# Performance work log

Hardware: AMD Instinct MI355X
Metric: run time of the kernel (lower is better)

## Reference

```python
import jax, jax.numpy as jnp
import numpy as np

DIM = 1024
NUM_HEADS = 16
HEAD_DIM = DIM // NUM_HEADS
EPS = 1e-5


def setup_inputs() -> dict:
    key = jax.random.key(0)
    ks = jax.random.split(key, 8)
    B, N = 4, 2048
    s = 0.02
    return {
        "x1": jax.random.normal(ks[0], (B, N, DIM), jnp.float32),
        "x2": jax.random.normal(ks[1], (B, N, DIM), jnp.float32),
        "wq": jax.random.normal(ks[2], (DIM, DIM), jnp.float32) * s,
        "bq": jnp.zeros((DIM,), jnp.float32),
        "wkv": jax.random.normal(ks[3], (DIM, 2 * DIM), jnp.float32) * s,
        "bkv": jnp.zeros((2 * DIM,), jnp.float32),
        "gamma_q": jnp.ones((HEAD_DIM,), jnp.float32),
        "beta_q": jnp.zeros((HEAD_DIM,), jnp.float32),
        "gamma_k": jnp.ones((HEAD_DIM,), jnp.float32),
        "beta_k": jnp.zeros((HEAD_DIM,), jnp.float32),
    }


def _layernorm(x, gamma, beta):
    m = jnp.mean(x, axis=-1, keepdims=True)
    v = jnp.mean(jnp.square(x - m), axis=-1, keepdims=True)
    return (x - m) * jax.lax.rsqrt(v + EPS) * gamma + beta


def reference(x1, x2, wq, bq, wkv, bkv, gamma_q, beta_q, gamma_k, beta_k):
    B, N, C = x1.shape
    H, D = NUM_HEADS, C // NUM_HEADS
    q = x1 @ wq + bq                      # [B,N,C]
    kv = x2 @ wkv + bkv                   # [B,N,2C]
    k, v = kv[..., :C], kv[..., C:]
    # [B,N,C] -> [B,H,N,D]
    q = q.reshape(B, N, H, D).transpose(0, 2, 1, 3)
    k = k.reshape(B, N, H, D).transpose(0, 2, 1, 3)
    v = v.reshape(B, N, H, D).transpose(0, 2, 1, 3)
    q = _layernorm(q, gamma_q, beta_q)
    k = _layernorm(k, gamma_k, beta_k)
    scale = 1.0 / jnp.sqrt(jnp.asarray(D, x1.dtype))
    scores = jnp.einsum("bhnd,bhmd->bhnm", q, k) * scale
    attn = jax.nn.softmax(scores, axis=-1)
    out = jnp.einsum("bhnm,bhmd->bhnd", attn, v)  # [B,H,N,D]
    return out.transpose(0, 2, 1, 3).reshape(B, N, C)
```

## Files before the change

### kernel.cpp

```cpp
#include <hip/hip_runtime.h>
#include <hip/hip_bf16.h>

#define NHEADS 16
#define HDIM 64
#define BATCH 4
#define SEQ 2048
#define CDIM 1024
#define ROWS (BATCH * SEQ)
#define QSCALE (0.125f * 1.44269504088896f)

typedef __attribute__((ext_vector_type(8))) short short8;
typedef __attribute__((ext_vector_type(4))) float f32x4;
typedef __attribute__((ext_vector_type(4))) unsigned int u32x4;
typedef __attribute__((ext_vector_type(2))) unsigned int u32x2;

__device__ inline short f2bf(float f) {
    unsigned int u = __builtin_bit_cast(unsigned int, f);
    unsigned int r = (u + 0x7fffu + ((u >> 16) & 1u)) >> 16;
    return (short)r;
}

__device__ __forceinline__ void gll16(const void* g, void* l) {
    __builtin_amdgcn_global_load_lds(
        (const __attribute__((address_space(1))) unsigned int*)g,
        (__attribute__((address_space(3))) unsigned int*)l, 16, 0, 0);
}

__device__ __forceinline__ unsigned int pack_bf2(float a, float b) {
    return __builtin_amdgcn_perm(__builtin_bit_cast(unsigned int, b),
                                 __builtin_bit_cast(unsigned int, a), 0x07060302u);
}

__global__ __launch_bounds__(256) void cvt_bf16(const float* __restrict__ src,
                                                short* __restrict__ dst, int n8) {
    int i = blockIdx.x * 256 + threadIdx.x;
    if (i < n8) {
        f32x4 a = ((const f32x4*)src)[i * 2];
        f32x4 b = ((const f32x4*)src)[i * 2 + 1];
        short8 o;
        o[0] = f2bf(a[0]); o[1] = f2bf(a[1]); o[2] = f2bf(a[2]); o[3] = f2bf(a[3]);
        o[4] = f2bf(b[0]); o[5] = f2bf(b[1]); o[6] = f2bf(b[2]); o[7] = f2bf(b[3]);
        ((short8*)dst)[i] = o;
    }
}

__global__ __launch_bounds__(256) void wtrans(const float* __restrict__ W,
                                              short* __restrict__ WT, int Nw) {
    __shared__ short T[64][72];
    const int t = threadIdx.x;
    const int n0 = blockIdx.x * 64, k0 = blockIdx.y * 64;
    const int kl = t >> 2, c4 = (t & 3) * 16;
    const float* src = W + (size_t)(k0 + kl) * Nw + n0 + c4;
    short8 s0, s1;
#pragma unroll
    for (int e = 0; e < 2; e++) {
        f32x4 u = *(const f32x4*)(src + e * 4);
        s0[e * 4 + 0] = f2bf(u[0]); s0[e * 4 + 1] = f2bf(u[1]);
        s0[e * 4 + 2] = f2bf(u[2]); s0[e * 4 + 3] = f2bf(u[3]);
        f32x4 v = *(const f32x4*)(src + 8 + e * 4);
        s1[e * 4 + 0] = f2bf(v[0]); s1[e * 4 + 1] = f2bf(v[1]);
        s1[e * 4 + 2] = f2bf(v[2]); s1[e * 4 + 3] = f2bf(v[3]);
    }
    *(short8*)&T[kl][c4] = s0;
    *(short8*)&T[kl][c4 + 8] = s1;
    __syncthreads();
#pragma unroll
    for (int pass = 0; pass < 2; pass++) {
        int n = (t >> 3) + pass * 32;
        short8 o;
#pragma unroll
        for (int e = 0; e < 8; e++) o[e] = T[(t & 7) * 8 + e][n];
        *(short8*)(WT + (size_t)(n0 + n) * 1024 + k0 + (t & 7) * 8) = o;
    }
}

__global__ __launch_bounds__(256) void gemm_fused(
    const short* __restrict__ A1,
    const short* __restrict__ A2,
    const short* __restrict__ WQT,
    const short* __restrict__ WKVT,
    const float* __restrict__ bq,
    const float* __restrict__ bkv,
    const float* __restrict__ gq, const float* __restrict__ btq,
    const float* __restrict__ gk, const float* __restrict__ btk,
    short* __restrict__ QOut,
    short* __restrict__ KOut,
    short* __restrict__ VT)
{
    __shared__ __align__(16) char smem[34816];
    short (*As)[32] = (short (*)[32])smem;
    short (*Bs)[32] = (short (*)[32])(smem + 8192);

    const int tid = threadIdx.x;
    const int wave = tid >> 6, lane = tid & 63;
    const int wr = wave >> 1, wc = wave & 1;
    const int quad = lane >> 4, l15 = lane & 15;

    const int lin = blockIdx.y * 24 + blockIdx.x;
    const int swz = (lin & 7) * 192 + (lin >> 3);
    const int rblk = swz / 24;
    const int cblkg = swz - rblk * 24;

    const bool isQ = cblkg < 8;
    const int cblk = isQ ? cblkg : cblkg - 8;
    const short* Ap = isQ ? A1 : A2;
    const short* BT = isQ ? WQT : WKVT;

    f32x4 acc[4][4];
#pragma unroll
    for (int i = 0; i < 4; i++)
#pragma unroll
        for (int j = 0; j < 4; j++) acc[i][j] = f32x4{0.f, 0.f, 0.f, 0.f};

    const int srow = wave * 32 + (lane >> 2);
    const int scol = (lane & 3) * 8;

    for (int k0 = 0; k0 < CDIM; k0 += 32) {
        __syncthreads();
#pragma unroll
        for (int c = 0; c < 2; c++) {
            gll16(Ap + (size_t)(rblk * 128 + srow + c * 16) * CDIM + k0 + scol,
                  &As[srow + c * 16][scol]);
            gll16(BT + (size_t)(cblk * 128 + srow + c * 16) * CDIM + k0 + scol,
                  &Bs[srow + c * 16][scol]);
        }
        __syncthreads();

        short8 af[4], bfr[4];
#pragma unroll
        for (int i = 0; i < 4; i++)
            af[i] = *(const short8*)&As[wr * 64 + i * 16 + l15][quad * 8];
#pragma unroll
        for (int j = 0; j < 4; j++)
            bfr[j] = *(const short8*)&Bs[wc * 64 + j * 16 + l15][quad * 8];
#pragma unroll
        for (int i = 0; i < 4; i++)
#pragma unroll
            for (int j = 0; j < 4; j++)
                acc[i][j] = __builtin_amdgcn_mfma_f32_16x16x32_bf16(af[i], bfr[j], acc[i][j], 0, 0, 0);
    }

    const int col0 = cblk * 128 + wc * 64;
    const int g = col0 >> 6;

    if (cblkg < 16) {
        const float* bias  = isQ ? bq : bkv;
        const float* gamma = isQ ? gq : gk;
        const float* beta  = isQ ? btq : btk;
        short* Out = isQ ? QOut : KOut;
        const float scale = isQ ? QSCALE : 1.f;
        const int h = g;
        float bv[4], gv[4], btv[4];
#pragma unroll
        for (int j = 0; j < 4; j++) {
            int d = j * 16 + l15;
            bv[j] = bias[col0 + d];
            gv[j] = gamma[d];
            btv[j] = beta[d];
        }
#pragma unroll
        for (int i = 0; i < 4; i++) {
            int rowl = rblk * 128 + wr * 64 + i * 16 + quad * 4;
#pragma unroll
            for (int reg = 0; reg < 4; reg++) {
                float x[4], s = 0.f, s2 = 0.f;
#pragma unroll
                for (int j = 0; j < 4; j++) {
                    x[j] = acc[i][j][reg] + bv[j];
                    s += x[j];
                    s2 += x[j] * x[j];
                }
#pragma unroll
                for (int m = 1; m < 16; m <<= 1) {
                    s += __shfl_xor(s, m);
                    s2 += __shfl_xor(s2, m);
                }
                float mean = s * (1.f / 64.f);
                float var = s2 * (1.f / 64.f) - mean * mean;
                float rstd = rsqrtf(var + 1e-5f);
                int r = rowl + reg;
                int b = r >> 11, n = r & (SEQ - 1);
                size_t base = (((size_t)b * NHEADS + h) * SEQ + n) * 64;
#pragma unroll
                for (int j = 0; j < 4; j++) {
                    float y = ((x[j] - mean) * rstd * gv[j] + btv[j]) * scale;
                    Out[base + j * 16 + l15] = f2bf(y);
                }
            }
        }
    } else {
        const int h = g - NHEADS;
        __syncthreads();
        short (*Ts)[64][68] = (short (*)[64][68])smem;
#pragma unroll
        for (int i = 0; i < 4; i++)
#pragma unroll
            for (int reg = 0; reg < 4; reg++)
#pragma unroll
                for (int j = 0; j < 4; j++)
                    Ts[wave][i * 16 + quad * 4 + reg][j * 16 + l15] =
                        f2bf(acc[i][j][reg] + bkv[col0 + j * 16 + l15]);
        const int r = rblk * 128 + wr * 64 + lane;
        const int b = r >> 11, n = r & (SEQ - 1);
        const size_t vtbase = (((size_t)b * NHEADS + h) * 64) * SEQ;
#pragma unroll
        for (int e8 = 0; e8 < 8; e8++) {
            short8 v = *(const short8*)&Ts[wave][lane][e8 * 8];
#pragma unroll
            for (int e = 0; e < 8; e++)
                VT[vtbase + (size_t)(e8 * 8 + e) * SEQ + n] = v[e];
        }
    }
}

template <int JD, bool FIRST>
__device__ __forceinline__ void band_store(float* __restrict__ Ot,
                                           const f32x4 (&o)[4][4],
                                           int l15, int q) {
#pragma unroll
    for (int qc = 0; qc < 4; qc++)
#pragma unroll
        for (int reg = 0; reg < 4; reg++) {
            float* dst = &Ot[(qc * 16 + l15) * 68 + JD * 16 + q * 4 + reg];
            if (FIRST) *dst = o[JD][qc][reg];
            else       *dst += o[JD][qc][reg];
        }
}

__global__ __launch_bounds__(256, 2) void attn_fa(
    const short* __restrict__ Q,
    const short* __restrict__ Kk,
    const short* __restrict__ VT,
    float* __restrict__ Out)
{
    __shared__ __align__(16) char smem_raw[20480];

    const int tid = threadIdx.x;
    const int w = tid >> 6, lane = tid & 63;
    const int q = lane >> 4, l15 = lane & 15;
    const int bh = blockIdx.x;
    const int b = bh >> 4, h = bh & 15;
    const int qt = blockIdx.y;
    const size_t hb = (size_t)bh * SEQ * 64;
    const size_t vb = (size_t)bh * 64 * SEQ;

    unsigned int* Pd = (unsigned int*)smem_raw + w * 1280;
    float* Ot = (float*)smem_raw;
    float* Lred = (float*)smem_raw + 64 * 68;

    short8 qf[4][2];
#pragma unroll
    for (int qc = 0; qc < 4; qc++)
#pragma unroll
        for (int dh = 0; dh < 2; dh++)
            qf[qc][dh] = *(const short8*)(Q + hb +
                (size_t)(qt * 64 + qc * 16 + l15) * 64 + dh * 32 + q * 8);

    short8 ones;
#pragma unroll
    for (int e = 0; e < 8; e++) ones[e] = (short)0x3F80;

    f32x4 o[4][4];
#pragma unroll
    for (int jd = 0; jd < 4; jd++)
#pragma unroll
        for (int qc = 0; qc < 4; qc++) o[jd][qc] = f32x4{0.f, 0.f, 0.f, 0.f};
    f32x4 osum[4];
#pragma unroll
    for (int qc = 0; qc < 4; qc++) osum[qc] = f32x4{0.f, 0.f, 0.f, 0.f};

    const short* kbase = Kk + hb + (size_t)(w * 32 + l15) * 64 + q * 8;
    const short* vbase = VT + vb + (size_t)l15 * SEQ + w * 32 + q * 8;

    for (int kti = 0; kti < 16; kti++) {
        short8 kf[2][2];
#pragma unroll
        for (int kt = 0; kt < 2; kt++)
#pragma unroll
            for (int dh = 0; dh < 2; dh++)
                kf[kt][dh] = *(const short8*)(kbase +
                    (size_t)(kti * 128 + kt * 16) * 64 + dh * 32);
        short8 vf[4];
#pragma unroll
        for (int jd = 0; jd < 4; jd++)
            vf[jd] = *(const short8*)(vbase + (size_t)(jd * 16) * SEQ + kti * 128);

#pragma unroll
        for (int kt = 0; kt < 2; kt++)
#pragma unroll
            for (int qc = 0; qc < 4; qc++) {
                f32x4 z = f32x4{0.f, 0.f, 0.f, 0.f};
                z = __builtin_amdgcn_mfma_f32_16x16x32_bf16(kf[kt][0], qf[qc][0], z, 0, 0, 0);
                z = __builtin_amdgcn_mfma_f32_16x16x32_bf16(kf[kt][1], qf[qc][1], z, 0, 0, 0);
                u32x2 d2;
                d2[0] = pack_bf2(__builtin_amdgcn_exp2f(z[0]), __builtin_amdgcn_exp2f(z[1]));
                d2[1] = pack_bf2(__builtin_amdgcn_exp2f(z[2]), __builtin_amdgcn_exp2f(z[3]));
                *(u32x2*)&Pd[(qc * 16 + l15) * 20 + kt * 8 + 2 * q] = d2;
            }

        short8 pf[4];
#pragma unroll
        for (int qc = 0; qc < 4; qc++) {
            u32x4 pr = *(const u32x4*)&Pd[(qc * 16 + l15) * 20 + 4 * q];
            pf[qc] = __builtin_bit_cast(short8, pr);
        }

#pragma unroll
        for (int qc = 0; qc < 4; qc++)
            osum[qc] = __builtin_amdgcn_mfma_f32_16x16x32_bf16(ones, pf[qc], osum[qc], 0, 0, 0);
#pragma unroll
        for (int jd = 0; jd < 4; jd++)
#pragma unroll
            for (int qc = 0; qc < 4; qc++)
                o[jd][qc] = __builtin_amdgcn_mfma_f32_16x16x32_bf16(vf[jd], pf[qc], o[jd][qc], 0, 0, 0);
    }

    __syncthreads();
#pragma unroll
    for (int p = 0; p < 4; p++) {
        const int jd = (w + p) & 3;
        if (p == 0) {
            switch (jd) {
            case 0: band_store<0, true>(Ot, o, l15, q); break;
            case 1: band_store<1, true>(Ot, o, l15, q); break;
            case 2: band_store<2, true>(Ot, o, l15, q); break;
            case 3: band_store<3, true>(Ot, o, l15, q); break;
            }
            if (q == 0) {
#pragma unroll
                for (int qc = 0; qc < 4; qc++)
                    Lred[w * 64 + qc * 16 + l15] = osum[qc][0];
            }
        } else {
            switch (jd) {
            case 0: band_store<0, false>(Ot, o, l15, q); break;
            case 1: band_store<1, false>(Ot, o, l15, q); break;
            case 2: band_store<2, false>(Ot, o, l15, q); break;
            case 3: band_store<3, false>(Ot, o, l15, q); break;
            }
        }
        __syncthreads();
    }

    const int row = tid >> 2, c = tid & 3;
    float l = Lred[row] + Lred[64 + row] + Lred[128 + row] + Lred[192 + row];
    float inv = 1.f / l;
    float* obase = Out + ((size_t)b * SEQ + qt * 64 + row) * CDIM + h * 64;
#pragma unroll
    for (int i = 0; i < 4; i++) {
        f32x4 t = *(const f32x4*)&Ot[row * 68 + (c + 4 * i) * 4];
        *(f32x4*)(obase + (c + 4 * i) * 4) = t * inv;
    }
}

extern "C" void kernel_launch(void* const* d_in, const int* in_sizes, int n_in,
                              void* d_out, int out_size, void* d_ws, size_t ws_size,
                              hipStream_t stream) {
    const float* x1 = (const float*)d_in[0];
    const float* x2 = (const float*)d_in[1];
    const float* wq = (const float*)d_in[2];
    const float* bq = (const float*)d_in[3];
    const float* wkv = (const float*)d_in[4];
    const float* bkv = (const float*)d_in[5];
    const float* gq = (const float*)d_in[6];
    const float* btq = (const float*)d_in[7];
    const float* gk = (const float*)d_in[8];
    const float* btk = (const float*)d_in[9];
    float* out = (float*)d_out;

    short* a1 = (short*)d_ws;
    short* a2 = a1 + (size_t)ROWS * CDIM;
    short* wqT = a2 + (size_t)ROWS * CDIM;
    short* wkvT = wqT + (size_t)CDIM * CDIM;
    short* qln = wkvT + (size_t)2 * CDIM * CDIM;
    short* kln = qln + (size_t)ROWS * CDIM;
    short* vt = kln + (size_t)ROWS * CDIM;

    const int n8 = ROWS * CDIM / 8;
    cvt_bf16<<<dim3(n8 / 256), 256, 0, stream>>>(x1, a1, n8);
    cvt_bf16<<<dim3(n8 / 256), 256, 0, stream>>>(x2, a2, n8);
    wtrans<<<dim3(16, 16), 256, 0, stream>>>(wq, wqT, CDIM);
    wtrans<<<dim3(32, 16), 256, 0, stream>>>(wkv, wkvT, 2 * CDIM);

    gemm_fused<<<dim3(24, 64), 256, 0, stream>>>(a1, a2, wqT, wkvT, bq, bkv,
                                                 gq, btq, gk, btk, qln, kln, vt);
    attn_fa<<<dim3(64, 32), 256, 0, stream>>>(qln, kln, vt, out);
}
```

Measured before the change: 371.0 us.

## Merge prep launches, remap GEMM blocks, software-pipeline attention K/V loads

Merges the two input conversions and the two weight transposes into single launches. It also gives the GEMM a 1D grid with separate swizzles for the Q and KV regions, and swizzles the attention block order so blocks sharing a head are scheduled together. The attention loop is software-pipelined: the next tile's K/V register fragments are prefetched while the current tile's MFMAs run, and the P buffer in LDS is double-buffered. This roughly doubles attention LDS use, which may reduce occupancy, and raises register pressure from the extra fragment buffers.

```diff
diff --git a/kernel.cpp b/kernel.cpp
--- a/kernel.cpp
+++ b/kernel.cpp
@@ -31,24 +31,35 @@
                                  __builtin_bit_cast(unsigned int, a), 0x07060302u);
 }
 
-__global__ __launch_bounds__(256) void cvt_bf16(const float* __restrict__ src,
-                                                short* __restrict__ dst, int n8) {
+__global__ __launch_bounds__(256) void cvt2_bf16(const float* __restrict__ s1,
+                                                 const float* __restrict__ s2,
+                                                 short* __restrict__ d1,
+                                                 short* __restrict__ d2, int n8each) {
     int i = blockIdx.x * 256 + threadIdx.x;
-    if (i < n8) {
-        f32x4 a = ((const f32x4*)src)[i * 2];
-        f32x4 b = ((const f32x4*)src)[i * 2 + 1];
-        short8 o;
-        o[0] = f2bf(a[0]); o[1] = f2bf(a[1]); o[2] = f2bf(a[2]); o[3] = f2bf(a[3]);
-        o[4] = f2bf(b[0]); o[5] = f2bf(b[1]); o[6] = f2bf(b[2]); o[7] = f2bf(b[3]);
-        ((short8*)dst)[i] = o;
-    }
-}
-
-__global__ __launch_bounds__(256) void wtrans(const float* __restrict__ W,
-                                              short* __restrict__ WT, int Nw) {
+    const float* src = s1;
+    short* dst = d1;
+    if (i >= n8each) { i -= n8each; src = s2; dst = d2; }
+    f32x4 a = ((const f32x4*)src)[i * 2];
+    f32x4 b = ((const f32x4*)src)[i * 2 + 1];
+    short8 o;
+    o[0] = f2bf(a[0]); o[1] = f2bf(a[1]); o[2] = f2bf(a[2]); o[3] = f2bf(a[3]);
+    o[4] = f2bf(b[0]); o[5] = f2bf(b[1]); o[6] = f2bf(b[2]); o[7] = f2bf(b[3]);
+    ((short8*)dst)[i] = o;
+}
+
+__global__ __launch_bounds__(256) void wtrans2(const float* __restrict__ Wq,
+                                               short* __restrict__ WQT,
+                                               const float* __restrict__ Wkv,
+                                               short* __restrict__ WKVT) {
     __shared__ short T[64][72];
     const int t = threadIdx.x;
-    const int n0 = blockIdx.x * 64, k0 = blockIdx.y * 64;
+    const int bx = blockIdx.x;
+    const float* W;
+    short* WT;
+    int Nw, n0;
+    if (bx < 16) { W = Wq;  WT = WQT;  Nw = 1024; n0 = bx * 64; }
+    else         { W = Wkv; WT = WKVT; Nw = 2048; n0 = (bx - 16) * 64; }
+    const int k0 = blockIdx.y * 64;
     const int kl = t >> 2, c4 = (t & 3) * 16;
     const float* src = W + (size_t)(k0 + kl) * Nw + n0 + c4;
     short8 s0, s1;
@@ -74,7 +85,7 @@
     }
 }
 
-__global__ __launch_bounds__(256) void gemm_fused(
+__global__ __launch_bounds__(256) void gemm_all(
     const short* __restrict__ A1,
     const short* __restrict__ A2,
     const short* __restrict__ WQT,
@@ -96,13 +107,17 @@
     const int wr = wave >> 1, wc = wave & 1;
     const int quad = lane >> 4, l15 = lane & 15;
 
-    const int lin = blockIdx.y * 24 + blockIdx.x;
-    const int swz = (lin & 7) * 192 + (lin >> 3);
-    const int rblk = swz / 24;
-    const int cblkg = swz - rblk * 24;
-
-    const bool isQ = cblkg < 8;
-    const int cblk = isQ ? cblkg : cblkg - 8;
+    const int lin = blockIdx.x;
+    const bool isQ = lin < 512;
+    int rblk, cblk;
+    if (isQ) {
+        const int swz = (lin & 7) * 64 + (lin >> 3);
+        rblk = swz >> 3; cblk = swz & 7;
+    } else {
+        const int kl = lin - 512;
+        const int swz = (kl & 7) * 128 + (kl >> 3);
+        rblk = swz >> 4; cblk = swz & 15;
+    }
     const short* Ap = isQ ? A1 : A2;
     const short* BT = isQ ? WQT : WKVT;
 
@@ -143,7 +158,7 @@
     const int col0 = cblk * 128 + wc * 64;
     const int g = col0 >> 6;
 
-    if (cblkg < 16) {
+    if (isQ || g < NHEADS) {
         const float* bias  = isQ ? bq : bkv;
         const float* gamma = isQ ? gq : gk;
         const float* beta  = isQ ? btq : btk;
@@ -227,24 +242,80 @@
         }
 }
 
+__device__ __forceinline__ void attn_body(
+    int t, bool doLoad,
+    const short* __restrict__ kbase, const short* __restrict__ vbase,
+    const short8 (&qf)[4][2], const short8& ones,
+    short8 (&kfCur)[2][2], short8 (&kfNxt)[2][2], short8 (&vfPN)[4],
+    unsigned int* __restrict__ PdW, unsigned int* __restrict__ PdR,
+    int l15, int q, f32x4 (&o)[4][4], f32x4 (&osum)[4])
+{
+    short8 pf[4];
+#pragma unroll
+    for (int qc = 0; qc < 4; qc++) {
+        u32x4 pr = *(const u32x4*)&PdR[(qc * 16 + l15) * 20 + 4 * q];
+        pf[qc] = __builtin_bit_cast(short8, pr);
+    }
+
+#pragma unroll
+    for (int kt = 0; kt < 2; kt++)
+#pragma unroll
+        for (int qc = 0; qc < 4; qc++) {
+            f32x4 z = f32x4{0.f, 0.f, 0.f, 0.f};
+            z = __builtin_amdgcn_mfma_f32_16x16x32_bf16(kfCur[kt][0], qf[qc][0], z, 0, 0, 0);
+            z = __builtin_amdgcn_mfma_f32_16x16x32_bf16(kfCur[kt][1], qf[qc][1], z, 0, 0, 0);
+            u32x2 d2;
+            d2[0] = pack_bf2(__builtin_amdgcn_exp2f(z[0]), __builtin_amdgcn_exp2f(z[1]));
+            d2[1] = pack_bf2(__builtin_amdgcn_exp2f(z[2]), __builtin_amdgcn_exp2f(z[3]));
+            *(u32x2*)&PdW[(qc * 16 + l15) * 20 + kt * 8 + 2 * q] = d2;
+        }
+
+    if (doLoad) {
+#pragma unroll
+        for (int kt = 0; kt < 2; kt++)
+#pragma unroll
+            for (int dh = 0; dh < 2; dh++)
+                kfNxt[kt][dh] = *(const short8*)(kbase +
+                    (size_t)((t + 1) * 128 + kt * 16) * 64 + dh * 32);
+    }
+
+#pragma unroll
+    for (int qc = 0; qc < 4; qc++)
+        osum[qc] = __builtin_amdgcn_mfma_f32_16x16x32_bf16(ones, pf[qc], osum[qc], 0, 0, 0);
+#pragma unroll
+    for (int jd = 0; jd < 4; jd++)
+#pragma unroll
+        for (int qc = 0; qc < 4; qc++)
+            o[jd][qc] = __builtin_amdgcn_mfma_f32_16x16x32_bf16(vfPN[jd], pf[qc], o[jd][qc], 0, 0, 0);
+
+    if (doLoad) {
+#pragma unroll
+        for (int jd = 0; jd < 4; jd++)
+            vfPN[jd] = *(const short8*)(vbase + (size_t)(jd * 16) * SEQ + (t + 1) * 128);
+    }
+}
+
 __global__ __launch_bounds__(256, 2) void attn_fa(
     const short* __restrict__ Q,
     const short* __restrict__ Kk,
     const short* __restrict__ VT,
     float* __restrict__ Out)
 {
-    __shared__ __align__(16) char smem_raw[20480];
+    __shared__ __align__(16) char smem_raw[40960];
 
     const int tid = threadIdx.x;
     const int w = tid >> 6, lane = tid & 63;
     const int q = lane >> 4, l15 = lane & 15;
-    const int bh = blockIdx.x;
+    const int lin = blockIdx.y * 64 + blockIdx.x;
+    const int swz = (lin & 7) * 256 + (lin >> 3);
+    const int bh = swz >> 5;
+    const int qt = swz & 31;
     const int b = bh >> 4, h = bh & 15;
-    const int qt = blockIdx.y;
     const size_t hb = (size_t)bh * SEQ * 64;
     const size_t vb = (size_t)bh * 64 * SEQ;
 
-    unsigned int* Pd = (unsigned int*)smem_raw + w * 1280;
+    unsigned int* PdA = (unsigned int*)smem_raw + w * 2560;
+    unsigned int* PdB = PdA + 1280;
     float* Ot = (float*)smem_raw;
     float* Lred = (float*)smem_raw + 64 * 68;
 
@@ -272,39 +343,50 @@
     const short* kbase = Kk + hb + (size_t)(w * 32 + l15) * 64 + q * 8;
     const short* vbase = VT + vb + (size_t)l15 * SEQ + w * 32 + q * 8;
 
-    for (int kti = 0; kti < 16; kti++) {
-        short8 kf[2][2];
-#pragma unroll
-        for (int kt = 0; kt < 2; kt++)
-#pragma unroll
-            for (int dh = 0; dh < 2; dh++)
-                kf[kt][dh] = *(const short8*)(kbase +
-                    (size_t)(kti * 128 + kt * 16) * 64 + dh * 32);
-        short8 vf[4];
-#pragma unroll
-        for (int jd = 0; jd < 4; jd++)
-            vf[jd] = *(const short8*)(vbase + (size_t)(jd * 16) * SEQ + kti * 128);
-
-#pragma unroll
-        for (int kt = 0; kt < 2; kt++)
-#pragma unroll
-            for (int qc = 0; qc < 4; qc++) {
-                f32x4 z = f32x4{0.f, 0.f, 0.f, 0.f};
-                z = __builtin_amdgcn_mfma_f32_16x16x32_bf16(kf[kt][0], qf[qc][0], z, 0, 0, 0);
-                z = __builtin_amdgcn_mfma_f32_16x16x32_bf16(kf[kt][1], qf[qc][1], z, 0, 0, 0);
-                u32x2 d2;
-                d2[0] = pack_bf2(__builtin_amdgcn_exp2f(z[0]), __builtin_amdgcn_exp2f(z[1]));
-                d2[1] = pack_bf2(__builtin_amdgcn_exp2f(z[2]), __builtin_amdgcn_exp2f(z[3]));
-                *(u32x2*)&Pd[(qc * 16 + l15) * 20 + kt * 8 + 2 * q] = d2;
-            }
-
+    short8 kfA[2][2], kfB[2][2], vfA[4], vfB[4];
+
+#pragma unroll
+    for (int kt = 0; kt < 2; kt++)
+#pragma unroll
+        for (int dh = 0; dh < 2; dh++)
+            kfA[kt][dh] = *(const short8*)(kbase + (size_t)(kt * 16) * 64 + dh * 32);
+#pragma unroll
+    for (int jd = 0; jd < 4; jd++)
+        vfA[jd] = *(const short8*)(vbase + (size_t)(jd * 16) * SEQ);
+#pragma unroll
+    for (int kt = 0; kt < 2; kt++)
+#pragma unroll
+        for (int qc = 0; qc < 4; qc++) {
+            f32x4 z = f32x4{0.f, 0.f, 0.f, 0.f};
+            z = __builtin_amdgcn_mfma_f32_16x16x32_bf16(kfA[kt][0], qf[qc][0], z, 0, 0, 0);
+            z = __builtin_amdgcn_mfma_f32_16x16x32_bf16(kfA[kt][1], qf[qc][1], z, 0, 0, 0);
+            u32x2 d2;
+            d2[0] = pack_bf2(__builtin_amdgcn_exp2f(z[0]), __builtin_amdgcn_exp2f(z[1]));
+            d2[1] = pack_bf2(__builtin_amdgcn_exp2f(z[2]), __builtin_amdgcn_exp2f(z[3]));
+            *(u32x2*)&PdA[(qc * 16 + l15) * 20 + kt * 8 + 2 * q] = d2;
+        }
+#pragma unroll
+    for (int kt = 0; kt < 2; kt++)
+#pragma unroll
+        for (int dh = 0; dh < 2; dh++)
+            kfB[kt][dh] = *(const short8*)(kbase + (size_t)(128 + kt * 16) * 64 + dh * 32);
+#pragma unroll
+    for (int jd = 0; jd < 4; jd++)
+        vfB[jd] = *(const short8*)(vbase + (size_t)(jd * 16) * SEQ + 128);
+
+    for (int t = 1; t < 15; t += 2) {
+        attn_body(t,     true, kbase, vbase, qf, ones, kfB, kfA, vfA, PdB, PdA, l15, q, o, osum);
+        attn_body(t + 1, true, kbase, vbase, qf, ones, kfA, kfB, vfB, PdA, PdB, l15, q, o, osum);
+    }
+    attn_body(15, false, kbase, vbase, qf, ones, kfB, kfA, vfA, PdB, PdA, l15, q, o, osum);
+
+    {
         short8 pf[4];
 #pragma unroll
         for (int qc = 0; qc < 4; qc++) {
-            u32x4 pr = *(const u32x4*)&Pd[(qc * 16 + l15) * 20 + 4 * q];
+            u32x4 pr = *(const u32x4*)&PdB[(qc * 16 + l15) * 20 + 4 * q];
             pf[qc] = __builtin_bit_cast(short8, pr);
         }
-
 #pragma unroll
         for (int qc = 0; qc < 4; qc++)
             osum[qc] = __builtin_amdgcn_mfma_f32_16x16x32_bf16(ones, pf[qc], osum[qc], 0, 0, 0);
@@ -312,7 +394,7 @@
         for (int jd = 0; jd < 4; jd++)
 #pragma unroll
             for (int qc = 0; qc < 4; qc++)
-                o[jd][qc] = __builtin_amdgcn_mfma_f32_16x16x32_bf16(vf[jd], pf[qc], o[jd][qc], 0, 0, 0);
+                o[jd][qc] = __builtin_amdgcn_mfma_f32_16x16x32_bf16(vfB[jd], pf[qc], o[jd][qc], 0, 0, 0);
     }
 
     __syncthreads();
@@ -377,12 +459,9 @@
     short* vt = kln + (size_t)ROWS * CDIM;
 
     const int n8 = ROWS * CDIM / 8;
-    cvt_bf16<<<dim3(n8 / 256), 256, 0, stream>>>(x1, a1, n8);
-    cvt_bf16<<<dim3(n8 / 256), 256, 0, stream>>>(x2, a2, n8);
-    wtrans<<<dim3(16, 16), 256, 0, stream>>>(wq, wqT, CDIM);
-    wtrans<<<dim3(32, 16), 256, 0, stream>>>(wkv, wkvT, 2 * CDIM);
-
-    gemm_fused<<<dim3(24, 64), 256, 0, stream>>>(a1, a2, wqT, wkvT, bq, bkv,
-                                                 gq, btq, gk, btk, qln, kln, vt);
+    cvt2_bf16<<<dim3(2 * n8 / 256), 256, 0, stream>>>(x1, x2, a1, a2, n8);
+    wtrans2<<<dim3(48, 16), 256, 0, stream>>>(wq, wqT, wkv, wkvT);
+    gemm_all<<<dim3(1536), 256, 0, stream>>>(a1, a2, wqT, wkvT, bq, bkv,
+                                             gq, btq, gk, btk, qln, kln, vt);
     attn_fa<<<dim3(64, 32), 256, 0, stream>>>(qln, kln, vt, out);
 }
```

New measurement: 330.7 us. 1.12x faster.
